# Kernel optimization log

Measured on AMD Instinct MI355X. Metric: run time of the kernel, lower is better.

Reference implementation:

```python
import jax, jax.numpy as jnp
import numpy as np

N_NODES = 100000
N_EDGES = 1000000
D_FEAT = 64
N_GRAPHS = 64


def setup_inputs() -> dict:
    key = jax.random.key(0)
    ks = jax.random.split(key, 5)
    x = jax.random.normal(ks[0], (N_NODES, D_FEAT), dtype=jnp.float32)
    edge_index = jax.random.randint(ks[1], (2, N_EDGES), 0, N_NODES, dtype=jnp.int32)
    batch = jnp.sort(jax.random.randint(ks[2], (N_NODES,), 0, N_GRAPHS, dtype=jnp.int32))
    s = 1.0 / np.sqrt(D_FEAT)
    W1 = jax.random.uniform(ks[3], (D_FEAT, D_FEAT), jnp.float32, -s, s)
    W2 = jax.random.uniform(ks[4], (D_FEAT, D_FEAT), jnp.float32, -s, s)
    b1 = jnp.zeros((D_FEAT,), jnp.float32)
    b2 = jnp.zeros((D_FEAT,), jnp.float32)
    return {"x": x, "edge_index": edge_index, "batch": batch,
            "W1": W1, "b1": b1, "W2": W2, "b2": b2}


def gcn_conv(x, edge_index, W, b, num_nodes):
    # PyG GCNConv: h = D^{-1/2} (A + I) D^{-1/2} (x W) + b
    loops = jnp.arange(num_nodes, dtype=edge_index.dtype)
    row = jnp.concatenate([edge_index[0], loops])  # source nodes
    col = jnp.concatenate([edge_index[1], loops])  # target nodes
    h = x @ W  # [N, D]
    deg = jax.ops.segment_sum(jnp.ones_like(col, dtype=h.dtype), col,
                              num_segments=num_nodes)  # >= 1 due to self loops
    dinv = jax.lax.rsqrt(deg)
    norm = dinv[row] * dinv[col]  # [E+N]
    out = jax.ops.segment_sum(h[row] * norm[:, None], col, num_segments=num_nodes)
    return out + b


def reference(x, edge_index, batch, W1, b1, W2, b2):
    n = x.shape[0]
    h = gcn_conv(x, edge_index, W1, b1, n)
    h = gcn_conv(h, edge_index, W2, b2, n)
    # global_mean_pool over graph ids
    sums = jax.ops.segment_sum(h, batch, num_segments=N_GRAPHS)  # [G, D]
    cnts = jax.ops.segment_sum(jnp.ones((n, 1), h.dtype), batch,
                               num_segments=N_GRAPHS)
    return sums / jnp.maximum(cnts, 1.0)
```

## Files before the change

### kernel.cpp

```cpp
#include <hip/hip_runtime.h>
#include <hip/hip_fp16.h>

#define DFEAT 64
#define NG 64
#define TILE 128
#define NBLK 256
#define NBMAX 1024
#define NREP 16

__global__ __launch_bounds__(256) void k_cnt(const int* __restrict__ col,
                                             int* __restrict__ cnt_m,
                                             int e, int nb, int chunk) {
  __shared__ int hist[NBMAX];
  int tid = threadIdx.x;
  int blk = blockIdx.x;
  for (int b = tid; b < nb; b += 256) hist[b] = 0;
  __syncthreads();
  int lo = blk * chunk, hi = min(lo + chunk, e);
  for (int i = lo + tid; i < hi; i += 256)
    atomicAdd(&hist[col[i] >> 7], 1);
  __syncthreads();
  for (int b = tid; b < nb; b += 256)
    cnt_m[(size_t)blk * nb + b] = hist[b];
}

__global__ __launch_bounds__(256) void k_colscan(int* __restrict__ cnt_m,
                                                 int* __restrict__ gcount, int nb) {
  __shared__ int sh[256];
  int tid = threadIdx.x;
  int b = blockIdx.x;
  int v = cnt_m[(size_t)tid * nb + b];
  sh[tid] = v;
  __syncthreads();
  for (int off = 1; off < 256; off <<= 1) {
    int t = (tid >= off) ? sh[tid - off] : 0;
    __syncthreads();
    sh[tid] += t;
    __syncthreads();
  }
  cnt_m[(size_t)tid * nb + b] = sh[tid] - v;
  if (tid == 255) gcount[b] = sh[255];
}

__global__ __launch_bounds__(1024) void k_bscan(const int* __restrict__ gcount,
                                                int* __restrict__ base, int nb) {
  __shared__ int sh[1024];
  int tid = threadIdx.x;
  int v = (tid < nb) ? gcount[tid] : 0;
  sh[tid] = v;
  __syncthreads();
  for (int off = 1; off < 1024; off <<= 1) {
    int t = (tid >= off) ? sh[tid - off] : 0;
    __syncthreads();
    sh[tid] += t;
    __syncthreads();
  }
  if (tid < nb) base[tid] = sh[tid] - v;
  if (tid == 0) base[nb] = sh[1023];
}

__global__ __launch_bounds__(256) void k_bin2(const int* __restrict__ row,
                                              const int* __restrict__ col,
                                              const int* __restrict__ base,
                                              const int* __restrict__ cnt_m,
                                              int* __restrict__ pairs,
                                              int e, int nb, int chunk) {
  __shared__ int gl[NBMAX];
  __shared__ int lcur[NBMAX];
  int tid = threadIdx.x;
  int blk = blockIdx.x;
  for (int b = tid; b < nb; b += 256) {
    gl[b] = base[b] + cnt_m[(size_t)blk * nb + b];
    lcur[b] = 0;
  }
  __syncthreads();
  int lo = blk * chunk, hi = min(lo + chunk, e);
  for (int i = lo + tid; i < hi; i += 256) {
    int s = row[i], t = col[i];
    int b = t >> 7;
    int pos = gl[b] + atomicAdd(&lcur[b], 1);
    pairs[pos] = s | ((t & (TILE - 1)) << 20);
  }
}

__global__ __launch_bounds__(256) void k_csr(const int* __restrict__ pairs,
                                             const int* __restrict__ base,
                                             const float* __restrict__ x,
                                             int* __restrict__ starts,
                                             int* __restrict__ srcs,
                                             float* __restrict__ dinv,
                                             __half2* __restrict__ xh,
                                             int n, int e) {
  __shared__ int cnt[TILE];
  __shared__ int cur[TILE];
  __shared__ int sc[TILE];
  __shared__ float sdv[TILE];
  int tid = threadIdx.x;
  int b = blockIdx.x;
  int tile0 = b * TILE;
  if (tid < TILE) cnt[tid] = 0;
  __syncthreads();
  int e0 = base[b], e1 = base[b + 1];
  for (int i = e0 + tid; i < e1; i += 256)
    atomicAdd(&cnt[(unsigned)pairs[i] >> 20], 1);
  __syncthreads();
  int c = (tid < TILE) ? cnt[tid] : 0;
  if (tid < TILE) sc[tid] = c;
  __syncthreads();
  for (int off = 1; off < TILE; off <<= 1) {
    int t = (tid < TILE && tid >= off) ? sc[tid - off] : 0;
    __syncthreads();
    if (tid < TILE) sc[tid] += t;
    __syncthreads();
  }
  if (tid < TILE) {
    int excl = sc[tid] - c;
    cur[tid] = excl;
    int node = tile0 + tid;
    float d = rsqrtf(1.0f + (float)c);
    sdv[tid] = (node < n) ? d : 0.f;
    if (node < n) {
      starts[node] = e0 + excl;
      dinv[node] = d;
    }
  }
  if (b == 0 && tid == 0) starts[n] = e;
  __syncthreads();
  for (int i = e0 + tid; i < e1; i += 256) {
    int p = pairs[i];
    int pos = atomicAdd(&cur[(unsigned)p >> 20], 1);
    srcs[e0 + pos] = p & 0xFFFFF;
  }
  int nnode = min(n - tile0, TILE);
  if (nnode > 0) {
    int nfl = nnode * 16;
    const float4* xf = (const float4*)(x + (size_t)tile0 * 64);
    float2* xo = (float2*)xh + (size_t)tile0 * 16;
    for (int p = tid; p < nfl; p += 256) {
      float4 v = xf[p];
      float d = sdv[p >> 4];
      float2 st;
      ((__half2*)&st)[0] = __floats2half2_rn(v.x * d, v.y * d);
      ((__half2*)&st)[1] = __floats2half2_rn(v.z * d, v.w * d);
      xo[p] = st;
    }
  }
}

__global__ __launch_bounds__(256) void k_w12(const float* __restrict__ W1,
                                             const float* __restrict__ W2,
                                             const float* __restrict__ b1,
                                             const int* __restrict__ batch,
                                             float* __restrict__ WW,
                                             float* __restrict__ bw,
                                             float* __restrict__ cntf, int n) {
  __shared__ float w1[4096], w2[4096];
  int tid = threadIdx.x;
  for (int i = tid; i < 4096; i += 256) { w1[i] = W1[i]; w2[i] = W2[i]; }
  if (tid < NG) {
    int g = tid;
    int lo = 0, hi = n;
    while (lo < hi) { int m = (lo + hi) >> 1; if (batch[m] < g) lo = m + 1; else hi = m; }
    int a = lo;
    lo = 0; hi = n;
    while (lo < hi) { int m = (lo + hi) >> 1; if (batch[m] < g + 1) lo = m + 1; else hi = m; }
    cntf[g] = (float)(lo - a);
  }
  __syncthreads();
  for (int p = tid; p < 4096; p += 256) {
    int k = p >> 6, d = p & 63;
    float a = 0.f;
    for (int m = 0; m < 64; ++m) a += w1[k * 64 + m] * w2[m * 64 + d];
    WW[p] = a;
  }
  if (tid < 64) {
    float a = 0.f;
    for (int k = 0; k < 64; ++k) a += b1[k] * w2[k * 64 + tid];
    bw[tid] = a;
  }
}

__device__ __forceinline__ void acc8w(float2& a0, float2& a1, float2& a2,
                                      float2& a3, float4 v, float w) {
  const __half2* hp = (const __half2*)&v;
  float2 t;
  t = __half22float2(hp[0]); a0.x = fmaf(w, t.x, a0.x); a0.y = fmaf(w, t.y, a0.y);
  t = __half22float2(hp[1]); a1.x = fmaf(w, t.x, a1.x); a1.y = fmaf(w, t.y, a1.y);
  t = __half22float2(hp[2]); a2.x = fmaf(w, t.x, a2.x); a2.y = fmaf(w, t.y, a2.y);
  t = __half22float2(hp[3]); a3.x = fmaf(w, t.x, a3.x); a3.y = fmaf(w, t.y, a3.y);
}
__device__ __forceinline__ void acc8(float2& a0, float2& a1, float2& a2,
                                     float2& a3, float4 v) {
  const __half2* hp = (const __half2*)&v;
  float2 t;
  t = __half22float2(hp[0]); a0.x += t.x; a0.y += t.y;
  t = __half22float2(hp[1]); a1.x += t.x; a1.y += t.y;
  t = __half22float2(hp[2]); a2.x += t.x; a2.y += t.y;
  t = __half22float2(hp[3]); a3.x += t.x; a3.y += t.y;
}

__global__ __launch_bounds__(256) void k_gather1(const int* __restrict__ starts,
                                                 const int* __restrict__ srcs,
                                                 const float* __restrict__ dinv,
                                                 const __half2* __restrict__ xh,
                                                 const int* __restrict__ batch,
                                                 __half2* __restrict__ z1h,
                                                 float* __restrict__ Tr, int n) {
  int tid = threadIdx.x;
  int node = blockIdx.x * 32 + (tid >> 3);
  bool act = node < n;
  int nc = act ? node : n - 1;
  int l = tid & 7;
  int lane = tid & 63;
  int rep = blockIdx.x & (NREP - 1);
  int s = starts[nc];
  int deg = act ? (starts[nc + 1] - s) : 0;
  float dc = dinv[nc];
  int g = batch[nc];
  const float4* xf = (const float4*)xh;
  float4 sv = xf[(size_t)nc * 8 + l];
  float2 a0 = make_float2(0.f, 0.f), a1 = a0, a2 = a0, a3 = a0;
  acc8(a0, a1, a2, a3, sv);
  float wsum = 0.f;
  int trips = (deg + 3) >> 2;
  int dm1 = deg - 1;
  int r0 = 0, r1 = 0, r2 = 0, r3 = 0;
  if (trips > 0) {
    r0 = srcs[s];
    r1 = srcs[s + min(1, dm1)];
    r2 = srcs[s + min(2, dm1)];
    r3 = srcs[s + min(3, dm1)];
  }
  int j = 0;
  for (int t = 0; t < trips; ++t) {
    int n0 = r0, n1 = r1, n2 = r2, n3 = r3;
    int jn = j + 4;
    r0 = srcs[s + min(jn + 0, dm1)];
    r1 = srcs[s + min(jn + 1, dm1)];
    r2 = srcs[s + min(jn + 2, dm1)];
    r3 = srcs[s + min(jn + 3, dm1)];
    float w1w = (j + 1 < deg) ? 1.f : 0.f;
    float w2w = (j + 2 < deg) ? 1.f : 0.f;
    float w3w = (j + 3 < deg) ? 1.f : 0.f;
    float4 v0 = xf[(size_t)n0 * 8 + l];
    float4 v1 = xf[(size_t)n1 * 8 + l];
    float4 v2 = xf[(size_t)n2 * 8 + l];
    float4 v3 = xf[(size_t)n3 * 8 + l];
    wsum += dinv[n0] + w1w * dinv[n1] + w2w * dinv[n2] + w3w * dinv[n3];
    acc8(a0, a1, a2, a3, v0);
    acc8w(a0, a1, a2, a3, v1, w1w);
    acc8w(a0, a1, a2, a3, v2, w2w);
    acc8w(a0, a1, a2, a3, v3, w3w);
    j = jn;
  }
  if (act) {
    float s2 = dc * dc;
    float4 ov;
    __half2* op = (__half2*)&ov;
    op[0] = __floats2half2_rn(s2 * a0.x, s2 * a0.y);
    op[1] = __floats2half2_rn(s2 * a1.x, s2 * a1.y);
    op[2] = __floats2half2_rn(s2 * a2.x, s2 * a2.y);
    op[3] = __floats2half2_rn(s2 * a3.x, s2 * a3.y);
    ((float4*)z1h)[(size_t)node * 8 + l] = ov;
  }
  float uval = act ? dc * (dc + wsum) : 0.f;
  int g0 = __shfl(g, 0);
  bool uni = (__all(g == g0) != 0);
  if (!uni) {
    if (act && l == 0) unsafeAtomicAdd(&Tr[rep * NG + g], uval);
  } else {
    float uv = (l == 0) ? uval : 0.f;
    uv += __shfl_xor(uv, 8);
    uv += __shfl_xor(uv, 16);
    uv += __shfl_xor(uv, 32);
    if (lane == 0 && uv != 0.f) unsafeAtomicAdd(&Tr[rep * NG + g0], uv);
  }
}

__global__ __launch_bounds__(256) void k_gather2(const int* __restrict__ starts,
                                                 const int* __restrict__ srcs,
                                                 const float* __restrict__ dinv,
                                                 const __half2* __restrict__ z1h,
                                                 const int* __restrict__ batch,
                                                 float* __restrict__ Pb,
                                                 float* __restrict__ S, int n) {
  __shared__ float rowacc[2][64];
  __shared__ int sgid[2];
  int tid = threadIdx.x;
  int blk0 = (int)blockIdx.x * 32;
  int node = blk0 + (tid >> 3);
  bool act = node < n;
  int nc = act ? node : n - 1;
  int l = tid & 7;
  int lane = tid & 63;
  int s = starts[nc];
  int deg = act ? (starts[nc + 1] - s) : 0;
  float dc = dinv[nc];
  int g = batch[nc];
  if (tid < 128) ((float*)rowacc)[tid] = 0.f;
  if (tid < 2) {
    int idx = blk0 + (tid ? 31 : 0);
    if (idx > n - 1) idx = n - 1;
    sgid[tid] = batch[idx];
  }
  const float4* xf = (const float4*)z1h;
  float4 sv = xf[(size_t)nc * 8 + l];
  float2 a0 = make_float2(0.f, 0.f), a1 = a0, a2 = a0, a3 = a0;
  acc8(a0, a1, a2, a3, sv);
  int trips = (deg + 3) >> 2;
  int dm1 = deg - 1;
  int r0 = 0, r1 = 0, r2 = 0, r3 = 0;
  if (trips > 0) {
    r0 = srcs[s];
    r1 = srcs[s + min(1, dm1)];
    r2 = srcs[s + min(2, dm1)];
    r3 = srcs[s + min(3, dm1)];
  }
  int j = 0;
  for (int t = 0; t < trips; ++t) {
    int n0 = r0, n1 = r1, n2 = r2, n3 = r3;
    int jn = j + 4;
    r0 = srcs[s + min(jn + 0, dm1)];
    r1 = srcs[s + min(jn + 1, dm1)];
    r2 = srcs[s + min(jn + 2, dm1)];
    r3 = srcs[s + min(jn + 3, dm1)];
    float w1w = (j + 1 < deg) ? 1.f : 0.f;
    float w2w = (j + 2 < deg) ? 1.f : 0.f;
    float w3w = (j + 3 < deg) ? 1.f : 0.f;
    float4 v0 = xf[(size_t)n0 * 8 + l];
    float4 v1 = xf[(size_t)n1 * 8 + l];
    float4 v2 = xf[(size_t)n2 * 8 + l];
    float4 v3 = xf[(size_t)n3 * 8 + l];
    acc8(a0, a1, a2, a3, v0);
    acc8w(a0, a1, a2, a3, v1, w1w);
    acc8w(a0, a1, a2, a3, v2, w2w);
    acc8w(a0, a1, a2, a3, v3, w3w);
    j = jn;
  }
  float f[8];
  f[0] = act ? dc * a0.x : 0.f;
  f[1] = act ? dc * a0.y : 0.f;
  f[2] = act ? dc * a1.x : 0.f;
  f[3] = act ? dc * a1.y : 0.f;
  f[4] = act ? dc * a2.x : 0.f;
  f[5] = act ? dc * a2.y : 0.f;
  f[6] = act ? dc * a3.x : 0.f;
  f[7] = act ? dc * a3.y : 0.f;
  __syncthreads();
  int g_lo = sgid[0], g_hi = sgid[1];
  int sel = (g == g_lo) ? 0 : ((g == g_hi) ? 1 : -1);
  if (sel < 0 && act) {
#pragma unroll
    for (int k = 0; k < 8; ++k)
      unsafeAtomicAdd(&S[g * 64 + l * 8 + k], f[k]);
  }
  float fa[8], fb[8];
#pragma unroll
  for (int k = 0; k < 8; ++k) {
    fa[k] = (sel == 0) ? f[k] : 0.f;
    fb[k] = (sel == 1) ? f[k] : 0.f;
  }
#pragma unroll
  for (int k = 0; k < 8; ++k) {
    fa[k] += __shfl_xor(fa[k], 8);
    fa[k] += __shfl_xor(fa[k], 16);
    fa[k] += __shfl_xor(fa[k], 32);
    fb[k] += __shfl_xor(fb[k], 8);
    fb[k] += __shfl_xor(fb[k], 16);
    fb[k] += __shfl_xor(fb[k], 32);
  }
  if (lane < 8) {
#pragma unroll
    for (int k = 0; k < 8; ++k) {
      if (fa[k] != 0.f) atomicAdd(&rowacc[0][lane * 8 + k], fa[k]);
      if (fb[k] != 0.f) atomicAdd(&rowacc[1][lane * 8 + k], fb[k]);
    }
  }
  __syncthreads();
  float* pb = Pb + (size_t)blockIdx.x * 130;
  if (tid < 128) pb[tid] = ((float*)rowacc)[tid];
  if (tid == 128) pb[128] = (float)g_lo;
  if (tid == 129) pb[129] = (float)g_hi;
}

__global__ __launch_bounds__(256) void k_sreduce(const float* __restrict__ Pb,
                                                 const int* __restrict__ batch,
                                                 float* __restrict__ S, int n) {
  __shared__ float sh[4][64];
  int g = blockIdx.x;
  int d = threadIdx.x & 63, r = threadIdx.x >> 6;
  int lo = 0, hi = n;
  while (lo < hi) { int m = (lo + hi) >> 1; if (batch[m] < g) lo = m + 1; else hi = m; }
  int a = lo;
  lo = 0; hi = n;
  while (lo < hi) { int m = (lo + hi) >> 1; if (batch[m] < g + 1) lo = m + 1; else hi = m; }
  int b = lo;
  float acc = 0.f;
  if (b > a) {
    int bl0 = a >> 5, bl1 = (b - 1) >> 5;
    for (int bl = bl0 + r; bl <= bl1; bl += 4) {
      const float* p = Pb + (size_t)bl * 130;
      if ((int)p[128] == g) acc += p[d];
      if ((int)p[129] == g) acc += p[64 + d];
    }
  }
  sh[r][d] = acc;
  __syncthreads();
  if (r == 0) S[g * 64 + d] += acc + sh[1][d] + sh[2][d] + sh[3][d];
}

__global__ __launch_bounds__(256) void k_final2(const float* __restrict__ S,
                                                const float* __restrict__ Tr,
                                                const float* __restrict__ cntf,
                                                const float* __restrict__ WW,
                                                const float* __restrict__ bw,
                                                const float* __restrict__ b2,
                                                float* __restrict__ out) {
  __shared__ float sS[4096], sW[4096], sT[64];
  int tid = threadIdx.x;
  for (int i = tid; i < 4096; i += 256) {
    sS[i] = S[i];
    sW[i] = WW[i];
  }
  if (tid < 64) {
    float t = 0.f;
    for (int r = 0; r < NREP; ++r) t += Tr[r * NG + tid];
    sT[tid] = t;
  }
  __syncthreads();
  for (int p = tid; p < 4096; p += 256) {
    int g = p >> 6, d = p & 63;
    float a = 0.f;
    for (int k = 0; k < 64; ++k) a += sS[g * 64 + k] * sW[k * 64 + d];
    float c = fmaxf(cntf[g], 1.0f);
    out[p] = (a + sT[g] * bw[d]) / c + b2[d];
  }
}

extern "C" void kernel_launch(void* const* d_in, const int* in_sizes, int n_in,
                              void* d_out, int out_size, void* d_ws, size_t ws_size,
                              hipStream_t stream) {
  const float* x = (const float*)d_in[0];
  const int* ei = (const int*)d_in[1];
  const int* bat = (const int*)d_in[2];
  const float* W1 = (const float*)d_in[3];
  const float* b1 = (const float*)d_in[4];
  const float* W2 = (const float*)d_in[5];
  const float* b2 = (const float*)d_in[6];
  float* out = (float*)d_out;

  int n = in_sizes[0] / 64;
  int e = in_sizes[1] / 2;
  const int* rowp = ei;
  const int* colp = ei + e;
  int nb = (n + TILE - 1) / TILE;
  int chunk = (e + NBLK - 1) / NBLK;
  int nbw = (n + 31) / 32;

  char* ws = (char*)d_ws;
  size_t off = 0;
  auto alloc = [&](size_t elems) {
    void* p = ws + off;
    off += ((elems * 4 + 255) & ~(size_t)255);
    return p;
  };
  float* S = (float*)alloc(NG * DFEAT);
  float* Tr = (float*)alloc(NREP * NG);
  float* cntf = (float*)alloc(NG);
  size_t zbytes = off;
  int* gcount = (int*)alloc(nb);
  int* base = (int*)alloc(nb + 1);
  int* cnt_m = (int*)alloc((size_t)NBLK * nb);
  float* dinv = (float*)alloc(n);
  int* starts = (int*)alloc(n + 1);
  int* srcs = (int*)alloc(e);
  float* WW = (float*)alloc(DFEAT * DFEAT);
  float* bw = (float*)alloc(DFEAT);
  __half2* xh = (__half2*)alloc((size_t)n * 32);
  __half2* z1h = (__half2*)alloc((size_t)n * 32);
  int* pairs = (int*)alloc(e);
  float* Pb = (float*)alloc((size_t)nbw * 130);

  (void)hipMemsetAsync(S, 0, zbytes, stream);
  k_cnt<<<NBLK, 256, 0, stream>>>(colp, cnt_m, e, nb, chunk);
  k_colscan<<<nb, 256, 0, stream>>>(cnt_m, gcount, nb);
  k_bscan<<<1, 1024, 0, stream>>>(gcount, base, nb);
  k_bin2<<<NBLK, 256, 0, stream>>>(rowp, colp, base, cnt_m, pairs, e, nb, chunk);
  k_csr<<<nb, 256, 0, stream>>>(pairs, base, x, starts, srcs, dinv, xh, n, e);
  k_w12<<<1, 256, 0, stream>>>(W1, W2, b1, bat, WW, bw, cntf, n);

  k_gather1<<<nbw, 256, 0, stream>>>(starts, srcs, dinv, xh, bat, z1h, Tr, n);
  k_gather2<<<nbw, 256, 0, stream>>>(starts, srcs, dinv, z1h, bat, Pb, S, n);
  k_sreduce<<<NG, 256, 0, stream>>>(Pb, bat, S, n);

  k_final2<<<1, 256, 0, stream>>>(S, Tr, cntf, WW, bw, b2, out);
}
```

Before: 213.9 us.

## Degree-sort nodes per tile for gathers, vectorize binning, merge small kernels

Several changes land together. The count and bin kernels now read edge indices with int4 loads, with the chunk size rounded to a multiple of four. The weight-product setup is folded into the scan launch as a second block. The CSR kernel builds a per-tile permutation of nodes sorted by degree bucket, which both gather kernels use so that the 8-lane groups in a wavefront have similar edge counts and diverge less. The S reduction and the final projection are fused into one 64-block kernel, which drops two launches but needs Pb bounds widened to whole tiles because nodes within a tile are now permuted.

```diff
diff --git a/kernel.cpp b/kernel.cpp
--- a/kernel.cpp
+++ b/kernel.cpp
@@ -7,6 +7,7 @@
 #define NBLK 256
 #define NBMAX 1024
 #define NREP 16
+#define SENT 0x7FFFFFFF
 
 __global__ __launch_bounds__(256) void k_cnt(const int* __restrict__ col,
                                              int* __restrict__ cnt_m,
@@ -17,8 +18,19 @@
   for (int b = tid; b < nb; b += 256) hist[b] = 0;
   __syncthreads();
   int lo = blk * chunk, hi = min(lo + chunk, e);
-  for (int i = lo + tid; i < hi; i += 256)
-    atomicAdd(&hist[col[i] >> 7], 1);
+  if (lo < hi) {
+    int nv = (hi - lo) >> 2;
+    const int4* c4 = (const int4*)(col + lo);
+    for (int i = tid; i < nv; i += 256) {
+      int4 v = c4[i];
+      atomicAdd(&hist[v.x >> 7], 1);
+      atomicAdd(&hist[v.y >> 7], 1);
+      atomicAdd(&hist[v.z >> 7], 1);
+      atomicAdd(&hist[v.w >> 7], 1);
+    }
+    for (int i = lo + (nv << 2) + tid; i < hi; i += 256)
+      atomicAdd(&hist[col[i] >> 7], 1);
+  }
   __syncthreads();
   for (int b = tid; b < nb; b += 256)
     cnt_m[(size_t)blk * nb + b] = hist[b];
@@ -43,20 +55,55 @@
 }
 
 __global__ __launch_bounds__(1024) void k_bscan(const int* __restrict__ gcount,
-                                                int* __restrict__ base, int nb) {
-  __shared__ int sh[1024];
-  int tid = threadIdx.x;
-  int v = (tid < nb) ? gcount[tid] : 0;
-  sh[tid] = v;
-  __syncthreads();
-  for (int off = 1; off < 1024; off <<= 1) {
-    int t = (tid >= off) ? sh[tid - off] : 0;
+                                                int* __restrict__ base, int nb,
+                                                const float* __restrict__ W1,
+                                                const float* __restrict__ W2,
+                                                const float* __restrict__ b1,
+                                                const int* __restrict__ batch,
+                                                float* __restrict__ WW,
+                                                float* __restrict__ bw,
+                                                float* __restrict__ cntf, int n) {
+  __shared__ float shm[8192];
+  int tid = threadIdx.x;
+  if (blockIdx.x == 0) {
+    int* sh = (int*)shm;
+    int v = (tid < nb) ? gcount[tid] : 0;
+    sh[tid] = v;
     __syncthreads();
-    sh[tid] += t;
+    for (int off = 1; off < 1024; off <<= 1) {
+      int t = (tid >= off) ? sh[tid - off] : 0;
+      __syncthreads();
+      sh[tid] += t;
+      __syncthreads();
+    }
+    if (tid < nb) base[tid] = sh[tid] - v;
+    if (tid == 0) base[nb] = sh[1023];
+  } else {
+    float* w1 = shm;
+    float* w2 = shm + 4096;
+    for (int i = tid; i < 4096; i += 1024) { w1[i] = W1[i]; w2[i] = W2[i]; }
+    if (tid < NG) {
+      int g = tid;
+      int lo = 0, hi = n;
+      while (lo < hi) { int m = (lo + hi) >> 1; if (batch[m] < g) lo = m + 1; else hi = m; }
+      int a = lo;
+      lo = 0; hi = n;
+      while (lo < hi) { int m = (lo + hi) >> 1; if (batch[m] < g + 1) lo = m + 1; else hi = m; }
+      cntf[g] = (float)(lo - a);
+    }
     __syncthreads();
-  }
-  if (tid < nb) base[tid] = sh[tid] - v;
-  if (tid == 0) base[nb] = sh[1023];
+    for (int p = tid; p < 4096; p += 1024) {
+      int k = p >> 6, d = p & 63;
+      float a = 0.f;
+      for (int m = 0; m < 64; ++m) a += w1[k * 64 + m] * w2[m * 64 + d];
+      WW[p] = a;
+    }
+    if (tid < 64) {
+      float a = 0.f;
+      for (int k = 0; k < 64; ++k) a += b1[k] * w2[k * 64 + tid];
+      bw[tid] = a;
+    }
+  }
 }
 
 __global__ __launch_bounds__(256) void k_bin2(const int* __restrict__ row,
@@ -75,7 +122,22 @@
   }
   __syncthreads();
   int lo = blk * chunk, hi = min(lo + chunk, e);
-  for (int i = lo + tid; i < hi; i += 256) {
+  if (lo >= hi) return;
+  int nv = (hi - lo) >> 2;
+  const int4* r4 = (const int4*)(row + lo);
+  const int4* c4 = (const int4*)(col + lo);
+  for (int i = tid; i < nv; i += 256) {
+    int4 rs = r4[i];
+    int4 ts = c4[i];
+#pragma unroll
+    for (int k = 0; k < 4; ++k) {
+      int s = (&rs.x)[k], t = (&ts.x)[k];
+      int b = t >> 7;
+      int pos = gl[b] + atomicAdd(&lcur[b], 1);
+      pairs[pos] = s | ((t & (TILE - 1)) << 20);
+    }
+  }
+  for (int i = lo + (nv << 2) + tid; i < hi; i += 256) {
     int s = row[i], t = col[i];
     int b = t >> 7;
     int pos = gl[b] + atomicAdd(&lcur[b], 1);
@@ -90,15 +152,18 @@
                                              int* __restrict__ srcs,
                                              float* __restrict__ dinv,
                                              __half2* __restrict__ xh,
+                                             int* __restrict__ order,
                                              int n, int e) {
   __shared__ int cnt[TILE];
   __shared__ int cur[TILE];
   __shared__ int sc[TILE];
   __shared__ float sdv[TILE];
+  __shared__ int dh[64], dcur[64];
   int tid = threadIdx.x;
   int b = blockIdx.x;
   int tile0 = b * TILE;
   if (tid < TILE) cnt[tid] = 0;
+  if (tid >= TILE && tid < TILE + 64) dh[tid - TILE] = 0;
   __syncthreads();
   int e0 = base[b], e1 = base[b + 1];
   for (int i = e0 + tid; i < e1; i += 256)
@@ -113,6 +178,7 @@
     if (tid < TILE) sc[tid] += t;
     __syncthreads();
   }
+  int mybin = 63;
   if (tid < TILE) {
     int excl = sc[tid] - c;
     cur[tid] = excl;
@@ -122,10 +188,22 @@
     if (node < n) {
       starts[node] = e0 + excl;
       dinv[node] = d;
-    }
+      mybin = min(c, 62);
+    }
+    atomicAdd(&dh[mybin], 1);
   }
   if (b == 0 && tid == 0) starts[n] = e;
   __syncthreads();
+  if (tid == 0) {
+    int a = 0;
+    for (int i = 0; i < 64; ++i) { int t = dh[i]; dcur[i] = a; a += t; }
+  }
+  __syncthreads();
+  if (tid < TILE) {
+    int rank = atomicAdd(&dcur[mybin], 1);
+    int node = tile0 + tid;
+    order[tile0 + rank] = (node < n) ? node : SENT;
+  }
   for (int i = e0 + tid; i < e1; i += 256) {
     int p = pairs[i];
     int pos = atomicAdd(&cur[(unsigned)p >> 20], 1);
@@ -147,39 +225,6 @@
   }
 }
 
-__global__ __launch_bounds__(256) void k_w12(const float* __restrict__ W1,
-                                             const float* __restrict__ W2,
-                                             const float* __restrict__ b1,
-                                             const int* __restrict__ batch,
-                                             float* __restrict__ WW,
-                                             float* __restrict__ bw,
-                                             float* __restrict__ cntf, int n) {
-  __shared__ float w1[4096], w2[4096];
-  int tid = threadIdx.x;
-  for (int i = tid; i < 4096; i += 256) { w1[i] = W1[i]; w2[i] = W2[i]; }
-  if (tid < NG) {
-    int g = tid;
-    int lo = 0, hi = n;
-    while (lo < hi) { int m = (lo + hi) >> 1; if (batch[m] < g) lo = m + 1; else hi = m; }
-    int a = lo;
-    lo = 0; hi = n;
-    while (lo < hi) { int m = (lo + hi) >> 1; if (batch[m] < g + 1) lo = m + 1; else hi = m; }
-    cntf[g] = (float)(lo - a);
-  }
-  __syncthreads();
-  for (int p = tid; p < 4096; p += 256) {
-    int k = p >> 6, d = p & 63;
-    float a = 0.f;
-    for (int m = 0; m < 64; ++m) a += w1[k * 64 + m] * w2[m * 64 + d];
-    WW[p] = a;
-  }
-  if (tid < 64) {
-    float a = 0.f;
-    for (int k = 0; k < 64; ++k) a += b1[k] * w2[k * 64 + tid];
-    bw[tid] = a;
-  }
-}
-
 __device__ __forceinline__ void acc8w(float2& a0, float2& a1, float2& a2,
                                       float2& a3, float4 v, float w) {
   const __half2* hp = (const __half2*)&v;
@@ -204,10 +249,12 @@
                                                  const float* __restrict__ dinv,
                                                  const __half2* __restrict__ xh,
                                                  const int* __restrict__ batch,
+                                                 const int* __restrict__ order,
                                                  __half2* __restrict__ z1h,
                                                  float* __restrict__ Tr, int n) {
   int tid = threadIdx.x;
-  int node = blockIdx.x * 32 + (tid >> 3);
+  int slot = blockIdx.x * 32 + (tid >> 3);
+  int node = order[slot];
   bool act = node < n;
   int nc = act ? node : n - 1;
   int l = tid & 7;
@@ -282,13 +329,15 @@
                                                  const float* __restrict__ dinv,
                                                  const __half2* __restrict__ z1h,
                                                  const int* __restrict__ batch,
+                                                 const int* __restrict__ order,
                                                  float* __restrict__ Pb,
                                                  float* __restrict__ S, int n) {
   __shared__ float rowacc[2][64];
   __shared__ int sgid[2];
   int tid = threadIdx.x;
   int blk0 = (int)blockIdx.x * 32;
-  int node = blk0 + (tid >> 3);
+  int slot = blk0 + (tid >> 3);
+  int node = order[slot];
   bool act = node < n;
   int nc = act ? node : n - 1;
   int l = tid & 7;
@@ -299,7 +348,8 @@
   int g = batch[nc];
   if (tid < 128) ((float*)rowacc)[tid] = 0.f;
   if (tid < 2) {
-    int idx = blk0 + (tid ? 31 : 0);
+    int tile0b = blk0 & ~(TILE - 1);
+    int idx = tile0b + (tid ? (TILE - 1) : 0);
     if (idx > n - 1) idx = n - 1;
     sgid[tid] = batch[idx];
   }
@@ -383,10 +433,18 @@
   if (tid == 129) pb[129] = (float)g_hi;
 }
 
-__global__ __launch_bounds__(256) void k_sreduce(const float* __restrict__ Pb,
-                                                 const int* __restrict__ batch,
-                                                 float* __restrict__ S, int n) {
+__global__ __launch_bounds__(256) void k_fin(const float* __restrict__ Pb,
+                                             const int* __restrict__ batch,
+                                             const float* __restrict__ S,
+                                             const float* __restrict__ Tr,
+                                             const float* __restrict__ cntf,
+                                             const float* __restrict__ WW,
+                                             const float* __restrict__ bw,
+                                             const float* __restrict__ b2,
+                                             float* __restrict__ out, int n,
+                                             int nbw) {
   __shared__ float sh[4][64];
+  __shared__ float sG[64];
   int g = blockIdx.x;
   int d = threadIdx.x & 63, r = threadIdx.x >> 6;
   int lo = 0, hi = n;
@@ -397,7 +455,8 @@
   int b = lo;
   float acc = 0.f;
   if (b > a) {
-    int bl0 = a >> 5, bl1 = (b - 1) >> 5;
+    int bl0 = (a >> 7) << 2;
+    int bl1 = min((((b - 1) >> 7) << 2) + 3, nbw - 1);
     for (int bl = bl0 + r; bl <= bl1; bl += 4) {
       const float* p = Pb + (size_t)bl * 130;
       if ((int)p[128] == g) acc += p[d];
@@ -406,34 +465,15 @@
   }
   sh[r][d] = acc;
   __syncthreads();
-  if (r == 0) S[g * 64 + d] += acc + sh[1][d] + sh[2][d] + sh[3][d];
-}
-
-__global__ __launch_bounds__(256) void k_final2(const float* __restrict__ S,
-                                                const float* __restrict__ Tr,
-                                                const float* __restrict__ cntf,
-                                                const float* __restrict__ WW,
-                                                const float* __restrict__ bw,
-                                                const float* __restrict__ b2,
-                                                float* __restrict__ out) {
-  __shared__ float sS[4096], sW[4096], sT[64];
-  int tid = threadIdx.x;
-  for (int i = tid; i < 4096; i += 256) {
-    sS[i] = S[i];
-    sW[i] = WW[i];
-  }
-  if (tid < 64) {
-    float t = 0.f;
-    for (int r = 0; r < NREP; ++r) t += Tr[r * NG + tid];
-    sT[tid] = t;
-  }
-  __syncthreads();
-  for (int p = tid; p < 4096; p += 256) {
-    int g = p >> 6, d = p & 63;
-    float a = 0.f;
-    for (int k = 0; k < 64; ++k) a += sS[g * 64 + k] * sW[k * 64 + d];
+  if (r == 0) sG[d] = acc + sh[1][d] + sh[2][d] + sh[3][d] + S[g * 64 + d];
+  __syncthreads();
+  if (threadIdx.x < 64) {
+    float aa = 0.f;
+    for (int k = 0; k < 64; ++k) aa += sG[k] * WW[k * 64 + d];
+    float T = 0.f;
+    for (int rr = 0; rr < NREP; ++rr) T += Tr[rr * NG + g];
     float c = fmaxf(cntf[g], 1.0f);
-    out[p] = (a + sT[g] * bw[d]) / c + b2[d];
+    out[g * 64 + d] = (aa + T * bw[d]) / c + b2[d];
   }
 }
 
@@ -454,7 +494,7 @@
   const int* rowp = ei;
   const int* colp = ei + e;
   int nb = (n + TILE - 1) / TILE;
-  int chunk = (e + NBLK - 1) / NBLK;
+  int chunk = (((e + NBLK - 1) / NBLK) + 3) & ~3;
   int nbw = (n + 31) / 32;
 
   char* ws = (char*)d_ws;
@@ -480,18 +520,21 @@
   __half2* z1h = (__half2*)alloc((size_t)n * 32);
   int* pairs = (int*)alloc(e);
   float* Pb = (float*)alloc((size_t)nbw * 130);
+  int* order = (int*)alloc((size_t)nb * TILE);
 
   (void)hipMemsetAsync(S, 0, zbytes, stream);
   k_cnt<<<NBLK, 256, 0, stream>>>(colp, cnt_m, e, nb, chunk);
   k_colscan<<<nb, 256, 0, stream>>>(cnt_m, gcount, nb);
-  k_bscan<<<1, 1024, 0, stream>>>(gcount, base, nb);
+  k_bscan<<<2, 1024, 0, stream>>>(gcount, base, nb, W1, W2, b1, bat, WW, bw,
+                                  cntf, n);
   k_bin2<<<NBLK, 256, 0, stream>>>(rowp, colp, base, cnt_m, pairs, e, nb, chunk);
-  k_csr<<<nb, 256, 0, stream>>>(pairs, base, x, starts, srcs, dinv, xh, n, e);
-  k_w12<<<1, 256, 0, stream>>>(W1, W2, b1, bat, WW, bw, cntf, n);
-
-  k_gather1<<<nbw, 256, 0, stream>>>(starts, srcs, dinv, xh, bat, z1h, Tr, n);
-  k_gather2<<<nbw, 256, 0, stream>>>(starts, srcs, dinv, z1h, bat, Pb, S, n);
-  k_sreduce<<<NG, 256, 0, stream>>>(Pb, bat, S, n);
-
-  k_final2<<<1, 256, 0, stream>>>(S, Tr, cntf, WW, bw, b2, out);
-}
+  k_csr<<<nb, 256, 0, stream>>>(pairs, base, x, starts, srcs, dinv, xh, order,
+                                n, e);
+
+  k_gather1<<<nbw, 256, 0, stream>>>(starts, srcs, dinv, xh, bat, order, z1h,
+                                     Tr, n);
+  k_gather2<<<nbw, 256, 0, stream>>>(starts, srcs, dinv, z1h, bat, order, Pb,
+                                     S, n);
+
+  k_fin<<<NG, 256, 0, stream>>>(Pb, bat, S, Tr, cntf, WW, bw, b2, out, n, nbw);
+}
```

Result: faster. 200.7 us (-6.2%).
